# Kernel optimization log

Hardware: AMD Instinct MI355X
Metric: run time of the kernel (lower is better)

## Reference

```python
import jax, jax.numpy as jnp
import numpy as np

N = 50000
E = 200000
IN = 165
HID = 100
H1, H2, H3 = 8, 8, 1
NC = 2
DIM1 = HID * H1  # 800
DIM2 = HID * H2  # 800
NEG_SLOPE = 0.2


def setup_inputs() -> dict:
    key = jax.random.key(0)
    ks = jax.random.split(key, 20)
    p = lambda k, shape: jax.random.normal(k, shape, jnp.float32) * 0.05
    x = jax.random.normal(ks[0], (N, IN), jnp.float32)
    edge_index = jax.random.randint(ks[1], (2, E), 0, N, jnp.int64)
    return {
        "x": x,
        "edge_index": edge_index,
        "W1": p(ks[2], (IN, H1 * HID)), "a1s": p(ks[3], (H1, HID)),
        "a1d": p(ks[4], (H1, HID)), "b1": jnp.zeros((H1 * HID,), jnp.float32),
        "W2": p(ks[5], (DIM1, H2 * HID)), "a2s": p(ks[6], (H2, HID)),
        "a2d": p(ks[7], (H2, HID)), "b2": jnp.zeros((H2 * HID,), jnp.float32),
        # gat3: 800 -> 2, 1 head, mean (concat=False)
        "W3": p(ks[8], (DIM2, H3 * NC)), "a3s": p(ks[9], (H3, NC)),
        "a3d": p(ks[10], (H3, NC)), "b3": jnp.zeros((NC,), jnp.float32),
        # residual / skip linears (bias=False), stored [in, out]
        "Wres1": p(ks[11], (DIM1, DIM2)),
        "Wres2": p(ks[12], (DIM2, NC)),
        "Wskip": p(ks[13], (IN, NC)),
    }


def gat_conv(x, W, a_src, a_dst, b, src, dst, n, heads, ch, concat):
    # h: [n, heads, ch] projected node features
    h = (x @ W).reshape(n, heads, ch)
    e_src = (h * a_src).sum(-1)  # [n, heads]
    e_dst = (h * a_dst).sum(-1)
    # per-edge attention logits, LeakyReLU as in PyG GATConv
    e = jax.nn.leaky_relu(e_src[src] + e_dst[dst], NEG_SLOPE)  # [Etot, heads]
    # segment softmax over incoming edges of each destination node
    m = jax.ops.segment_max(e, dst, num_segments=n)
    ex = jnp.exp(e - m[dst])
    denom = jax.ops.segment_sum(ex, dst, num_segments=n)
    alpha = ex / (denom[dst] + 1e-16)
    # weighted scatter-aggregation of source messages
    out = jax.ops.segment_sum(alpha[:, :, None] * h[src], dst, num_segments=n)
    out = out.reshape(n, heads * ch) if concat else out.mean(axis=1)
    return out + b


def reference(x, edge_index, W1, a1s, a1d, b1, W2, a2s, a2d, b2,
              W3, a3s, a3d, b3, Wres1, Wres2, Wskip):
    n = x.shape[0]
    loop = jnp.arange(n, dtype=edge_index.dtype)  # PyG adds self-loops by default
    src = jnp.concatenate([edge_index[0], loop])
    dst = jnp.concatenate([edge_index[1], loop])

    h1 = jax.nn.elu(gat_conv(x, W1, a1s, a1d, b1, src, dst, n, H1, HID, True))
    h2 = gat_conv(h1, W2, a2s, a2d, b2, src, dst, n, H2, HID, True) + h1 @ Wres1
    h2 = jax.nn.elu(h2)
    logits = gat_conv(h2, W3, a3s, a3d, b3, src, dst, n, H3, NC, False)
    logits = logits + h2 @ Wres2 + x @ Wskip
    return logits
```

## Files before the change

kernel.cpp:

```cpp
#include <hip/hip_runtime.h>

#define NN     50000
#define NE     200000
#define ETOT   250000
#define FIN    165
#define KP1    192
#define HEADS  8
#define CH     100
#define DIM    800
#define MPAD   50048
#define NP1    896
#define DIM2   1600
#define NP2    1664
#define NEG    0.2f

typedef unsigned short u16;
typedef unsigned int   u32;
typedef __bf16 bf16x8 __attribute__((ext_vector_type(8)));
typedef float  f32x4  __attribute__((ext_vector_type(4)));

__device__ __forceinline__ u16 f2b(float f) {
  u32 u = __float_as_uint(f);
  u = (u + 0x7FFFu + ((u >> 16) & 1u)) >> 16;
  return (u16)u;
}
__device__ __forceinline__ float b2f(u16 u) { return __uint_as_float(((u32)u) << 16); }

__global__ void k_count(const int* __restrict__ ei, int* __restrict__ cnt) {
  int e = blockIdx.x * 256 + threadIdx.x;
  if (e >= ETOT) return;
  int d = (e < NE) ? ei[NE + e] : (e - NE);
  atomicAdd(&cnt[d], 1);
}
__global__ void k_bsum(const int* __restrict__ cnt, int* __restrict__ bs) {
  __shared__ int sm[256];
  int i = blockIdx.x * 256 + threadIdx.x;
  sm[threadIdx.x] = (i < NN) ? cnt[i] : 0;
  __syncthreads();
  for (int off = 128; off; off >>= 1) {
    if (threadIdx.x < off) sm[threadIdx.x] += sm[threadIdx.x + off];
    __syncthreads();
  }
  if (!threadIdx.x) bs[blockIdx.x] = sm[0];
}
__global__ void k_top(int* __restrict__ bs, int* __restrict__ rs, int nb) {
  __shared__ int sm[256];
  int t = threadIdx.x;
  int v = (t < nb) ? bs[t] : 0;
  sm[t] = v; __syncthreads();
  for (int off = 1; off < 256; off <<= 1) {
    int add = (t >= off) ? sm[t - off] : 0;
    __syncthreads();
    sm[t] += add;
    __syncthreads();
  }
  if (t < nb) bs[t] = sm[t] - v;
  if (!t) rs[NN] = ETOT;
}
__global__ void k_scan(const int* __restrict__ cnt, const int* __restrict__ bs, int* __restrict__ rs) {
  __shared__ int sm[256];
  int t = threadIdx.x, i = blockIdx.x * 256 + t;
  int v = (i < NN) ? cnt[i] : 0;
  sm[t] = v; __syncthreads();
  for (int off = 1; off < 256; off <<= 1) {
    int add = (t >= off) ? sm[t - off] : 0;
    __syncthreads();
    sm[t] += add;
    __syncthreads();
  }
  if (i < NN) rs[i] = bs[blockIdx.x] + sm[t] - v;
}
__global__ void k_fill(const int* __restrict__ ei, const int* __restrict__ rs,
                       int* __restrict__ cur, int* __restrict__ esrc) {
  int e = blockIdx.x * 256 + threadIdx.x;
  if (e >= ETOT) return;
  int s, d;
  if (e < NE) { s = ei[e]; d = ei[NE + e]; } else { s = d = e - NE; }
  int pos = atomicAdd(&cur[d], 1);
  esrc[rs[d] + pos] = s;
}

__global__ void k_cvt_x(const float* __restrict__ x, u16* __restrict__ A) {
  int idx = blockIdx.x * 256 + threadIdx.x;
  int r = idx / KP1, k = idx - r * KP1;
  float v = (r < NN && k < FIN) ? x[r * FIN + k] : 0.f;
  A[idx] = f2b(v);
}
__global__ void k_cvt_w1(const float* __restrict__ W1, u16* __restrict__ Bt) {
  int idx = blockIdx.x * 256 + threadIdx.x;
  int j = idx / KP1, k = idx - j * KP1;
  float v = (j < DIM && k < FIN) ? W1[k * DIM + j] : 0.f;
  Bt[idx] = f2b(v);
}
__global__ void k_cvt_w2(const float* __restrict__ W2, const float* __restrict__ Wr1,
                         u16* __restrict__ Bt) {
  int idx = blockIdx.x * 256 + threadIdx.x;
  int j = idx / DIM, k = idx - j * DIM;
  float v = 0.f;
  if (j < DIM) v = W2[k * DIM + j];
  else if (j < 2 * DIM) v = Wr1[k * DIM + (j - DIM)];
  Bt[idx] = f2b(v);
}
__global__ void k_wa(const float* __restrict__ W, const float* __restrict__ as,
                     const float* __restrict__ ad, u16* __restrict__ Wt,
                     int Kin, int Kpad, int Dsp) {
  int idx = blockIdx.x * 256 + threadIdx.x;
  if (idx >= 16 * Kpad) return;
  int j = idx / Kpad, k = idx - j * Kpad;
  int h = j & 7;
  const float* a = ((j < 8) ? as : ad) + h * CH;
  float s = 0.f;
  if (k < Kin) {
    const float* wr = W + (size_t)k * DIM + h * CH;
    for (int c = 0; c < CH; ++c) s += wr[c] * a[c];
  }
  Wt[(size_t)(Dsp + j) * Kpad + k] = f2b(s);
}

__device__ __forceinline__ void gl_lds16(const u16* g, u16* l) {
  __builtin_amdgcn_global_load_lds((const __attribute__((address_space(1))) void*)g,
                                   (__attribute__((address_space(3))) void*)l, 16, 0, 0);
}
#define WAITVM(N) asm volatile("s_waitcnt vmcnt(" #N ")" ::: "memory")

__global__ __launch_bounds__(256) void k_gemm(const u16* __restrict__ A, const u16* __restrict__ Bt,
                                              u16* __restrict__ C, float* __restrict__ es,
                                              float* __restrict__ ed, int ksteps, int K,
                                              int Dsplit, int Nreal, int ldC) {
  __shared__ __align__(16) u16 lA[3][128 * 32];
  __shared__ __align__(16) u16 lB[3][128 * 32];
  int t = threadIdx.x;
  int lane = t & 63, wv = t >> 6;

  int nwg = gridDim.x * gridDim.y;
  int h = blockIdx.y * gridDim.x + blockIdx.x;
  int q = nwg >> 3, r8 = nwg & 7;
  int xcd = h & 7, i8 = h >> 3;
  int ln = (xcd < r8 ? xcd * (q + 1) : r8 * (q + 1) + (xcd - r8) * q) + i8;
  int tn = (ln % gridDim.x) * 128, tm = (ln / gridDim.x) * 128;

  int wr = (wv >> 1) * 64, wc = (wv & 1) * 64;
  int rl = lane & 15, kl = (lane >> 4) * 8;
  int srow = t >> 2, scb = (t & 3) * 8;

  f32x4 acc[4][4];
#pragma unroll
  for (int i = 0; i < 4; ++i)
#pragma unroll
    for (int j = 0; j < 4; ++j) acc[i][j] = (f32x4){0.f, 0.f, 0.f, 0.f};

  auto stage = [&](int buf, int ks) {
    int k0 = ks * 32;
    gl_lds16(A  + (size_t)(tm + srow) * K + k0 + scb,       &lA[buf][t * 8]);
    gl_lds16(A  + (size_t)(tm + srow + 64) * K + k0 + scb,  &lA[buf][(256 + t) * 8]);
    gl_lds16(Bt + (size_t)(tn + srow) * K + k0 + scb,       &lB[buf][t * 8]);
    gl_lds16(Bt + (size_t)(tn + srow + 64) * K + k0 + scb,  &lB[buf][(256 + t) * 8]);
  };

  stage(0, 0);
  if (ksteps > 1) stage(1, 1);
  int cur = 0;
  for (int ks = 0; ks < ksteps; ++ks) {
    if (ks + 1 < ksteps) { WAITVM(4); } else { WAITVM(0); }
    __builtin_amdgcn_s_barrier();
    if (ks + 2 < ksteps) {
      int sb = (cur == 0) ? 2 : cur - 1;
      stage(sb, ks + 2);
    }
    bf16x8 af[4], bfr[4];
#pragma unroll
    for (int i = 0; i < 4; ++i) {
      af[i]  = *(const bf16x8*)&lA[cur][(wr + i * 16 + rl) * 32 + kl];
      bfr[i] = *(const bf16x8*)&lB[cur][(wc + i * 16 + rl) * 32 + kl];
    }
    __builtin_amdgcn_s_setprio(1);
#pragma unroll
    for (int i = 0; i < 4; ++i)
#pragma unroll
      for (int j = 0; j < 4; ++j)
        acc[i][j] = __builtin_amdgcn_mfma_f32_16x16x32_bf16(af[i], bfr[j], acc[i][j], 0, 0, 0);
    __builtin_amdgcn_s_setprio(0);
    cur = (cur == 2) ? 0 : cur + 1;
  }
  int rq = (lane >> 4) * 4;
#pragma unroll
  for (int i = 0; i < 4; ++i) {
#pragma unroll
    for (int j = 0; j < 4; ++j) {
      int col = tn + wc + j * 16 + rl;
      if (col < Dsplit) {
#pragma unroll
        for (int q2 = 0; q2 < 4; ++q2) {
          int row = tm + wr + i * 16 + rq + q2;
          C[(size_t)row * ldC + col] = f2b(acc[i][j][q2]);
        }
      } else if (col < Nreal) {
        int cj = col - Dsplit;
        float* dst = (cj < 8) ? es : ed;
        int hh = cj & 7;
#pragma unroll
        for (int q2 = 0; q2 < 4; ++q2) {
          int row = tm + wr + i * 16 + rq + q2;
          dst[(size_t)row * 8 + hh] = acc[i][j][q2];
        }
      }
    }
  }
}

__global__ void k_stats(const int* __restrict__ rs, const int* __restrict__ esrc,
                        const float* __restrict__ es, const float* __restrict__ ed,
                        float* __restrict__ ex, float* __restrict__ dv) {
  int idx = blockIdx.x * 256 + threadIdx.x;
  if (idx >= NN * HEADS) return;
  int n = idx >> 3, h = idx & 7;
  int beg = rs[n], end = rs[n + 1];
  float edv = ed[idx];
  float den = 0.f;
  for (int j = beg; j < end; ++j) {
    float x = es[esrc[j] * 8 + h] + edv;
    x = x > 0.f ? x : NEG * x;
    float e = __expf(x);
    ex[j * 8 + h] = e;
    den += e;
  }
  dv[idx] = 1.f / (den + 1e-16f);
}

template <int LAYER>
__global__ __launch_bounds__(256) void k_agg(const int* __restrict__ rs, const int* __restrict__ esrc,
    const u16* __restrict__ Hp, const float* __restrict__ ex, const float* __restrict__ dv,
    const float* __restrict__ bias, const u16* __restrict__ resid, u16* __restrict__ out) {
  const int ld = (LAYER == 2) ? DIM2 : DIM;
  int n = blockIdx.x, t = threadIdx.x;
  if (t >= 200) return;
  int beg = rs[n], end = rs[n + 1];
  int c = t * 4;
  int h = t / 25;
  float inv = dv[n * 8 + h];
  float a0 = 0.f, a1 = 0.f, a2 = 0.f, a3 = 0.f;
  for (int j = beg; j < end; ++j) {
    int s = esrc[j];
    float w = ex[j * 8 + h];
    ushort4 u = *(const ushort4*)(Hp + (size_t)s * ld + c);
    a0 += w * b2f(u.x); a1 += w * b2f(u.y); a2 += w * b2f(u.z); a3 += w * b2f(u.w);
  }
  const float4 bb = *(const float4*)(bias + c);
  float v0 = a0 * inv + bb.x, v1 = a1 * inv + bb.y, v2 = a2 * inv + bb.z, v3 = a3 * inv + bb.w;
  if (LAYER == 2) {
    ushort4 r = *(const ushort4*)(resid + (size_t)n * DIM2 + c);
    v0 += b2f(r.x); v1 += b2f(r.y); v2 += b2f(r.z); v3 += b2f(r.w);
  }
  v0 = v0 > 0.f ? v0 : __expf(v0) - 1.f;
  v1 = v1 > 0.f ? v1 : __expf(v1) - 1.f;
  v2 = v2 > 0.f ? v2 : __expf(v2) - 1.f;
  v3 = v3 > 0.f ? v3 : __expf(v3) - 1.f;
  ushort4 o;
  o.x = f2b(v0); o.y = f2b(v1); o.z = f2b(v2); o.w = f2b(v3);
  *(ushort4*)(out + (size_t)n * DIM + c) = o;
}

__global__ __launch_bounds__(256) void k_l3(const u16* __restrict__ h2, const float* __restrict__ x,
    const float* __restrict__ W3, const float* __restrict__ Wres2, const float* __restrict__ Wskip,
    const float* __restrict__ a3s, const float* __restrict__ a3d, const float* __restrict__ b3,
    float* __restrict__ H3p, float* __restrict__ base, float* __restrict__ es3, float* __restrict__ ed3) {
  int wv = threadIdx.x >> 6, lane = threadIdx.x & 63;
  int n = blockIdx.x * 4 + wv;
  if (n >= NN) return;
  float p0 = 0.f, p1 = 0.f, r0 = 0.f, r1 = 0.f;
  const u16* hr = h2 + (size_t)n * DIM;
  for (int c = lane; c < DIM; c += 64) {
    float v = b2f(hr[c]);
    p0 += v * W3[2 * c];    p1 += v * W3[2 * c + 1];
    r0 += v * Wres2[2 * c]; r1 += v * Wres2[2 * c + 1];
  }
  float s0 = 0.f, s1 = 0.f;
  const float* xr = x + (size_t)n * FIN;
  for (int c = lane; c < FIN; c += 64) {
    float v = xr[c];
    s0 += v * Wskip[2 * c]; s1 += v * Wskip[2 * c + 1];
  }
#pragma unroll
  for (int off = 32; off; off >>= 1) {
    p0 += __shfl_down(p0, off); p1 += __shfl_down(p1, off);
    r0 += __shfl_down(r0, off); r1 += __shfl_down(r1, off);
    s0 += __shfl_down(s0, off); s1 += __shfl_down(s1, off);
  }
  if (!lane) {
    H3p[2 * n] = p0; H3p[2 * n + 1] = p1;
    es3[n] = p0 * a3s[0] + p1 * a3s[1];
    ed3[n] = p0 * a3d[0] + p1 * a3d[1];
    base[2 * n]     = r0 + s0 + b3[0];
    base[2 * n + 1] = r1 + s1 + b3[1];
  }
}

__global__ void k_l3agg(const int* __restrict__ rs, const int* __restrict__ esrc,
                        const float* __restrict__ H3p, const float* __restrict__ base,
                        const float* __restrict__ es3, const float* __restrict__ ed3,
                        float* __restrict__ out) {
  int n = blockIdx.x * 256 + threadIdx.x;
  if (n >= NN) return;
  int beg = rs[n], end = rs[n + 1];
  float edv = ed3[n];
  float den = 0.f, a0 = 0.f, a1 = 0.f;
  for (int j = beg; j < end; ++j) {
    int s = esrc[j];
    float e = es3[s] + edv;
    e = e > 0.f ? e : NEG * e;
    float exv = __expf(e);
    den += exv;
    a0 += exv * H3p[2 * s];
    a1 += exv * H3p[2 * s + 1];
  }
  float inv = 1.f / (den + 1e-16f);
  out[2 * n]     = base[2 * n]     + a0 * inv;
  out[2 * n + 1] = base[2 * n + 1] + a1 * inv;
}

extern "C" void kernel_launch(void* const* d_in, const int* in_sizes, int n_in,
                              void* d_out, int out_size, void* d_ws, size_t ws_size,
                              hipStream_t stream) {
  (void)in_sizes; (void)n_in; (void)out_size; (void)ws_size;
  const float* x    = (const float*)d_in[0];
  const int*   ei   = (const int*)d_in[1];
  const float* W1   = (const float*)d_in[2];
  const float* a1s  = (const float*)d_in[3];
  const float* a1d  = (const float*)d_in[4];
  const float* b1   = (const float*)d_in[5];
  const float* W2   = (const float*)d_in[6];
  const float* a2s  = (const float*)d_in[7];
  const float* a2d  = (const float*)d_in[8];
  const float* b2   = (const float*)d_in[9];
  const float* W3   = (const float*)d_in[10];
  const float* a3s  = (const float*)d_in[11];
  const float* a3d  = (const float*)d_in[12];
  const float* b3   = (const float*)d_in[13];
  const float* Wr1  = (const float*)d_in[14];
  const float* Wr2  = (const float*)d_in[15];
  const float* Wsk  = (const float*)d_in[16];
  float* out = (float*)d_out;

  char* w = (char*)d_ws;
  size_t off = 0;
  auto alloc = [&](size_t bytes) { void* p = w + off; off += (bytes + 255) & ~(size_t)255; return p; };
  int* cnt   = (int*)alloc((size_t)NN * 4);
  int* cur   = (int*)alloc((size_t)NN * 4);
  int* rs    = (int*)alloc((size_t)(NN + 1) * 4);
  int* bs    = (int*)alloc(256 * 4);
  int* esrc  = (int*)alloc((size_t)ETOT * 4);
  float* es  = (float*)alloc((size_t)MPAD * HEADS * 4);
  float* ed  = (float*)alloc((size_t)MPAD * HEADS * 4);
  float* exb = (float*)alloc((size_t)ETOT * HEADS * 4);
  float* dvf = (float*)alloc((size_t)NN * HEADS * 4);
  u16* W1t   = (u16*)alloc((size_t)NP1 * KP1 * 2);
  u16* W2t   = (u16*)alloc((size_t)NP2 * DIM * 2);
  float* H3p = (float*)alloc((size_t)NN * 2 * 4);
  float* base= (float*)alloc((size_t)NN * 2 * 4);
  float* es3 = (float*)alloc((size_t)NN * 4);
  float* ed3 = (float*)alloc((size_t)NN * 4);
  u16* bufB  = (u16*)alloc((size_t)MPAD * DIM * 2);
  u16* bufA  = (u16*)alloc((size_t)MPAD * DIM2 * 2);
  u16* H1p   = bufA;
  u16* G2    = bufA;
  u16* A1    = bufA + (size_t)MPAD * DIM;

  const int nb = (NN + 255) / 256;
  const int ge = (ETOT + 255) / 256;
  const int gh = (NN * HEADS + 255) / 256;

  hipMemsetAsync(cnt, 0, (size_t)NN * 4, stream);
  hipMemsetAsync(cur, 0, (size_t)NN * 4, stream);
  k_count<<<ge, 256, 0, stream>>>(ei, cnt);
  k_bsum <<<nb, 256, 0, stream>>>(cnt, bs);
  k_top  <<<1, 256, 0, stream>>>(bs, rs, nb);
  k_scan <<<nb, 256, 0, stream>>>(cnt, bs, rs);
  k_fill <<<ge, 256, 0, stream>>>(ei, rs, cur, esrc);

  k_cvt_x <<<(MPAD * KP1) / 256, 256, 0, stream>>>(x, A1);
  k_cvt_w1<<<(NP1 * KP1) / 256, 256, 0, stream>>>(W1, W1t);
  k_wa    <<<(16 * KP1 + 255) / 256, 256, 0, stream>>>(W1, a1s, a1d, W1t, FIN, KP1, DIM);
  k_cvt_w2<<<(NP2 * DIM) / 256, 256, 0, stream>>>(W2, Wr1, W2t);
  k_wa    <<<(16 * DIM + 255) / 256, 256, 0, stream>>>(W2, a2s, a2d, W2t, DIM, DIM, DIM2);

  k_gemm<<<dim3(NP1 / 128, MPAD / 128), 256, 0, stream>>>(A1, W1t, H1p, es, ed,
                                                          KP1 / 32, KP1, DIM, DIM + 16, DIM);
  k_stats<<<gh, 256, 0, stream>>>(rs, esrc, es, ed, exb, dvf);
  k_agg<1><<<NN, 256, 0, stream>>>(rs, esrc, H1p, exb, dvf, b1, (const u16*)nullptr, bufB);

  k_gemm<<<dim3(NP2 / 128, MPAD / 128), 256, 0, stream>>>(bufB, W2t, G2, es, ed,
                                                          DIM / 32, DIM, DIM2, DIM2 + 16, DIM2);
  k_stats<<<gh, 256, 0, stream>>>(rs, esrc, es, ed, exb, dvf);
  k_agg<2><<<NN, 256, 0, stream>>>(rs, esrc, G2, exb, dvf, b2, G2 + DIM, bufB);

  k_l3   <<<(NN + 3) / 4, 256, 0, stream>>>(bufB, x, W3, Wr2, Wsk, a3s, a3d, b3, H3p, base, es3, ed3);
  k_l3agg<<<nb, 256, 0, stream>>>(rs, esrc, H3p, base, es3, ed3, out);
}
```

Measured before the change: 561.4 us.

## Replace 128x128 GEMM with 256x256 tile, 512-thread, swizzled LDS kernel

The bf16 MFMA GEMM moves from 128x128 tiles with K=32 steps and triple buffering to 256x256 tiles with 8 waves, K=64 steps and double buffering. The LDS layout is XOR-swizzled to avoid bank conflicts. Padding changes to fit the larger tiles: M goes to 50176, N to 1024/1792, and layer-2 K to 832. The workspace is reorganised, with row guards on stores, aliased buffers, and the layer-1 aggregation output written with the padded stride. The aim is more data reuse per tile and fewer LDS and global loads per MFMA, at the cost of more padded wasted compute and lower occupancy.

Measured after the change: 597.7 us. 6.5% more time.

```diff
diff --git a/kernel.cpp b/kernel.cpp
--- a/kernel.cpp
+++ b/kernel.cpp
@@ -8,10 +8,11 @@
 #define HEADS  8
 #define CH     100
 #define DIM    800
-#define MPAD   50048
-#define NP1    896
+#define MPAD   50176
+#define NP1    1024
 #define DIM2   1600
-#define NP2    1664
+#define KP2    832
+#define NP2    1792
 #define NEG    0.2f
 
 typedef unsigned short u16;
@@ -88,17 +89,18 @@
 }
 __global__ void k_cvt_w1(const float* __restrict__ W1, u16* __restrict__ Bt) {
   int idx = blockIdx.x * 256 + threadIdx.x;
+  if (idx >= DIM * KP1) return;
   int j = idx / KP1, k = idx - j * KP1;
-  float v = (j < DIM && k < FIN) ? W1[k * DIM + j] : 0.f;
+  float v = (k < FIN) ? W1[k * DIM + j] : 0.f;
   Bt[idx] = f2b(v);
 }
 __global__ void k_cvt_w2(const float* __restrict__ W2, const float* __restrict__ Wr1,
                          u16* __restrict__ Bt) {
   int idx = blockIdx.x * 256 + threadIdx.x;
-  int j = idx / DIM, k = idx - j * DIM;
+  if (idx >= DIM2 * KP2) return;
+  int j = idx / KP2, k = idx - j * KP2;
   float v = 0.f;
-  if (j < DIM) v = W2[k * DIM + j];
-  else if (j < 2 * DIM) v = Wr1[k * DIM + (j - DIM)];
+  if (k < DIM) v = (j < DIM) ? W2[k * DIM + j] : Wr1[k * DIM + (j - DIM)];
   Bt[idx] = f2b(v);
 }
 __global__ void k_wa(const float* __restrict__ W, const float* __restrict__ as,
@@ -123,76 +125,104 @@
 }
 #define WAITVM(N) asm volatile("s_waitcnt vmcnt(" #N ")" ::: "memory")
 
-__global__ __launch_bounds__(256) void k_gemm(const u16* __restrict__ A, const u16* __restrict__ Bt,
-                                              u16* __restrict__ C, float* __restrict__ es,
-                                              float* __restrict__ ed, int ksteps, int K,
-                                              int Dsplit, int Nreal, int ldC) {
-  __shared__ __align__(16) u16 lA[3][128 * 32];
-  __shared__ __align__(16) u16 lB[3][128 * 32];
-  int t = threadIdx.x;
-  int lane = t & 63, wv = t >> 6;
+__global__ __launch_bounds__(512, 2) void k_gemm256(
+    const u16* __restrict__ A, const u16* __restrict__ Bt, u16* __restrict__ C,
+    float* __restrict__ es, float* __restrict__ ed,
+    int Kpad, int NT, int Dsplit, int Nreal, int ldC, int Mreal) {
+  __shared__ __align__(16) u16 lA[2][16384];
+  __shared__ __align__(16) u16 lB[2][16384];
+  const int t = threadIdx.x;
+  const int lane = t & 63, w = t >> 6;
+  const int wm = w >> 2, wn = w & 3;
 
   int nwg = gridDim.x * gridDim.y;
-  int h = blockIdx.y * gridDim.x + blockIdx.x;
+  int hid = blockIdx.y * gridDim.x + blockIdx.x;
   int q = nwg >> 3, r8 = nwg & 7;
-  int xcd = h & 7, i8 = h >> 3;
+  int xcd = hid & 7, i8 = hid >> 3;
   int ln = (xcd < r8 ? xcd * (q + 1) : r8 * (q + 1) + (xcd - r8) * q) + i8;
-  int tn = (ln % gridDim.x) * 128, tm = (ln / gridDim.x) * 128;
-
-  int wr = (wv >> 1) * 64, wc = (wv & 1) * 64;
-  int rl = lane & 15, kl = (lane >> 4) * 8;
-  int srow = t >> 2, scb = (t & 3) * 8;
-
-  f32x4 acc[4][4];
-#pragma unroll
-  for (int i = 0; i < 4; ++i)
+  int tn = (ln % gridDim.x) * 256, tm = (ln / gridDim.x) * 256;
+
+  const int srow = ((w >> 1) << 4) + (lane >> 2);
+  const int scol = ((w & 1) << 5) + (((lane & 3) * 8) ^ (((lane >> 5) & 1) << 4));
+  const size_t rA = (size_t)(tm + srow) * Kpad + scol;
+  const size_t rB = (size_t)(tn + srow) * Kpad + scol;
+  const size_t oR = (size_t)64 * Kpad;
+  const int dul = w * 512 + lane * 8;
+
+  f32x4 acc[8][4];
+#pragma unroll
+  for (int i = 0; i < 8; ++i)
 #pragma unroll
     for (int j = 0; j < 4; ++j) acc[i][j] = (f32x4){0.f, 0.f, 0.f, 0.f};
 
-  auto stage = [&](int buf, int ks) {
-    int k0 = ks * 32;
-    gl_lds16(A  + (size_t)(tm + srow) * K + k0 + scb,       &lA[buf][t * 8]);
-    gl_lds16(A  + (size_t)(tm + srow + 64) * K + k0 + scb,  &lA[buf][(256 + t) * 8]);
-    gl_lds16(Bt + (size_t)(tn + srow) * K + k0 + scb,       &lB[buf][t * 8]);
-    gl_lds16(Bt + (size_t)(tn + srow + 64) * K + k0 + scb,  &lB[buf][(256 + t) * 8]);
+  auto issue = [&](int buf, int kt) {
+    const u16* pa = A + rA + (size_t)kt * 64;
+    gl_lds16(pa,          &lA[buf][dul]);
+    gl_lds16(pa + oR,     &lA[buf][4096 + dul]);
+    gl_lds16(pa + 2 * oR, &lA[buf][8192 + dul]);
+    gl_lds16(pa + 3 * oR, &lA[buf][12288 + dul]);
+    const u16* pb = Bt + rB + (size_t)kt * 64;
+    gl_lds16(pb,          &lB[buf][dul]);
+    gl_lds16(pb + oR,     &lB[buf][4096 + dul]);
+    gl_lds16(pb + 2 * oR, &lB[buf][8192 + dul]);
+    gl_lds16(pb + 3 * oR, &lB[buf][12288 + dul]);
   };
 
-  stage(0, 0);
-  if (ksteps > 1) stage(1, 1);
-  int cur = 0;
-  for (int ks = 0; ks < ksteps; ++ks) {
-    if (ks + 1 < ksteps) { WAITVM(4); } else { WAITVM(0); }
+  const int rl = lane & 15, kl = (lane >> 4) * 8;
+  const int rdoff = rl * 32 + (kl ^ (((rl >> 3) & 1) << 4));
+
+  issue(0, 0);
+  if (NT > 1) issue(1, 1);
+  WAITVM(8);
+  __builtin_amdgcn_s_barrier();
+
+  for (int kt = 0; kt < NT; ++kt) {
+    const int buf = kt & 1;
+    const u16* baseA = &lA[buf][wm * 8192];
+    const u16* baseB = &lB[buf][(wn >> 1) * 8192];
+    bf16x8 b[4][2];
+#pragma unroll
+    for (int fc = 0; fc < 4; ++fc)
+#pragma unroll
+      for (int kk = 0; kk < 2; ++kk)
+        b[fc][kk] = *(const bf16x8*)&baseB[((((wn & 1) * 4 + fc) * 2 + kk) << 9) + rdoff];
+#pragma unroll
+    for (int qm = 0; qm < 2; ++qm) {
+      bf16x8 a[4][2];
+#pragma unroll
+      for (int i = 0; i < 4; ++i)
+#pragma unroll
+        for (int kk = 0; kk < 2; ++kk)
+          a[i][kk] = *(const bf16x8*)&baseA[((((qm * 4 + i) * 2) + kk) << 9) + rdoff];
+      __builtin_amdgcn_s_setprio(1);
+#pragma unroll
+      for (int i = 0; i < 4; ++i)
+#pragma unroll
+        for (int fc = 0; fc < 4; ++fc)
+#pragma unroll
+          for (int kk = 0; kk < 2; ++kk)
+            acc[qm * 4 + i][fc] =
+                __builtin_amdgcn_mfma_f32_16x16x32_bf16(a[i][kk], b[fc][kk], acc[qm * 4 + i][fc], 0, 0, 0);
+      __builtin_amdgcn_s_setprio(0);
+    }
     __builtin_amdgcn_s_barrier();
-    if (ks + 2 < ksteps) {
-      int sb = (cur == 0) ? 2 : cur - 1;
-      stage(sb, ks + 2);
-    }
-    bf16x8 af[4], bfr[4];
-#pragma unroll
-    for (int i = 0; i < 4; ++i) {
-      af[i]  = *(const bf16x8*)&lA[cur][(wr + i * 16 + rl) * 32 + kl];
-      bfr[i] = *(const bf16x8*)&lB[cur][(wc + i * 16 + rl) * 32 + kl];
-    }
-    __builtin_amdgcn_s_setprio(1);
-#pragma unroll
-    for (int i = 0; i < 4; ++i)
-#pragma unroll
-      for (int j = 0; j < 4; ++j)
-        acc[i][j] = __builtin_amdgcn_mfma_f32_16x16x32_bf16(af[i], bfr[j], acc[i][j], 0, 0, 0);
-    __builtin_amdgcn_s_setprio(0);
-    cur = (cur == 2) ? 0 : cur + 1;
-  }
-  int rq = (lane >> 4) * 4;
-#pragma unroll
-  for (int i = 0; i < 4; ++i) {
-#pragma unroll
-    for (int j = 0; j < 4; ++j) {
-      int col = tn + wc + j * 16 + rl;
+    if (kt + 2 < NT) { issue(buf, kt + 2); WAITVM(8); }
+    else             { WAITVM(0); }
+    __builtin_amdgcn_s_barrier();
+    __builtin_amdgcn_sched_barrier(0);
+  }
+
+  const int rq = (lane >> 4) * 4;
+#pragma unroll
+  for (int fr = 0; fr < 8; ++fr) {
+#pragma unroll
+    for (int fc = 0; fc < 4; ++fc) {
+      int col = tn + wn * 64 + fc * 16 + rl;
       if (col < Dsplit) {
 #pragma unroll
         for (int q2 = 0; q2 < 4; ++q2) {
-          int row = tm + wr + i * 16 + rq + q2;
-          C[(size_t)row * ldC + col] = f2b(acc[i][j][q2]);
+          int row = tm + wm * 128 + fr * 16 + rq + q2;
+          if (row < Mreal) C[(size_t)row * ldC + col] = f2b(acc[fr][fc][q2]);
         }
       } else if (col < Nreal) {
         int cj = col - Dsplit;
@@ -200,8 +230,8 @@
         int hh = cj & 7;
 #pragma unroll
         for (int q2 = 0; q2 < 4; ++q2) {
-          int row = tm + wr + i * 16 + rq + q2;
-          dst[(size_t)row * 8 + hh] = acc[i][j][q2];
+          int row = tm + wm * 128 + fr * 16 + rq + q2;
+          if (row < Mreal) dst[(size_t)row * 8 + hh] = acc[fr][fc][q2];
         }
       }
     }
@@ -231,7 +261,8 @@
 __global__ __launch_bounds__(256) void k_agg(const int* __restrict__ rs, const int* __restrict__ esrc,
     const u16* __restrict__ Hp, const float* __restrict__ ex, const float* __restrict__ dv,
     const float* __restrict__ bias, const u16* __restrict__ resid, u16* __restrict__ out) {
-  const int ld = (LAYER == 2) ? DIM2 : DIM;
+  const int ld  = (LAYER == 2) ? DIM2 : DIM;
+  const int old = (LAYER == 1) ? KP2 : DIM;
   int n = blockIdx.x, t = threadIdx.x;
   if (t >= 200) return;
   int beg = rs[n], end = rs[n + 1];
@@ -241,9 +272,9 @@
   float a0 = 0.f, a1 = 0.f, a2 = 0.f, a3 = 0.f;
   for (int j = beg; j < end; ++j) {
     int s = esrc[j];
-    float w = ex[j * 8 + h];
+    float wv = ex[j * 8 + h];
     ushort4 u = *(const ushort4*)(Hp + (size_t)s * ld + c);
-    a0 += w * b2f(u.x); a1 += w * b2f(u.y); a2 += w * b2f(u.z); a3 += w * b2f(u.w);
+    a0 += wv * b2f(u.x); a1 += wv * b2f(u.y); a2 += wv * b2f(u.z); a3 += wv * b2f(u.w);
   }
   const float4 bb = *(const float4*)(bias + c);
   float v0 = a0 * inv + bb.x, v1 = a1 * inv + bb.y, v2 = a2 * inv + bb.z, v3 = a3 * inv + bb.w;
@@ -257,7 +288,7 @@
   v3 = v3 > 0.f ? v3 : __expf(v3) - 1.f;
   ushort4 o;
   o.x = f2b(v0); o.y = f2b(v1); o.z = f2b(v2); o.w = f2b(v3);
-  *(ushort4*)(out + (size_t)n * DIM + c) = o;
+  *(ushort4*)(out + (size_t)n * old + c) = o;
 }
 
 __global__ __launch_bounds__(256) void k_l3(const u16* __restrict__ h2, const float* __restrict__ x,
@@ -349,21 +380,21 @@
   int* rs    = (int*)alloc((size_t)(NN + 1) * 4);
   int* bs    = (int*)alloc(256 * 4);
   int* esrc  = (int*)alloc((size_t)ETOT * 4);
-  float* es  = (float*)alloc((size_t)MPAD * HEADS * 4);
-  float* ed  = (float*)alloc((size_t)MPAD * HEADS * 4);
+  float* es  = (float*)alloc((size_t)NN * HEADS * 4);
+  float* ed  = (float*)alloc((size_t)NN * HEADS * 4);
   float* exb = (float*)alloc((size_t)ETOT * HEADS * 4);
   float* dvf = (float*)alloc((size_t)NN * HEADS * 4);
-  u16* W1t   = (u16*)alloc((size_t)NP1 * KP1 * 2);
-  u16* W2t   = (u16*)alloc((size_t)NP2 * DIM * 2);
-  float* H3p = (float*)alloc((size_t)NN * 2 * 4);
-  float* base= (float*)alloc((size_t)NN * 2 * 4);
-  float* es3 = (float*)alloc((size_t)NN * 4);
-  float* ed3 = (float*)alloc((size_t)NN * 4);
-  u16* bufB  = (u16*)alloc((size_t)MPAD * DIM * 2);
-  u16* bufA  = (u16*)alloc((size_t)MPAD * DIM2 * 2);
+  u16* W2t   = (u16*)alloc((size_t)NP2 * KP2 * 2);
+  u16* bufB  = (u16*)alloc((size_t)MPAD * KP2 * 2);
+  u16* bufA  = (u16*)alloc((size_t)NN * DIM2 * 2);
   u16* H1p   = bufA;
+  u16* A1    = bufA + (size_t)NN * DIM;
+  u16* W1t   = A1 + (size_t)MPAD * KP1;
   u16* G2    = bufA;
-  u16* A1    = bufA + (size_t)MPAD * DIM;
+  float* H3p  = exb;
+  float* base = exb + 2 * NN;
+  float* es3  = exb + 4 * NN;
+  float* ed3  = exb + 5 * NN;
 
   const int nb = (NN + 255) / 256;
   const int ge = (ETOT + 255) / 256;
@@ -378,18 +409,18 @@
   k_fill <<<ge, 256, 0, stream>>>(ei, rs, cur, esrc);
 
   k_cvt_x <<<(MPAD * KP1) / 256, 256, 0, stream>>>(x, A1);
-  k_cvt_w1<<<(NP1 * KP1) / 256, 256, 0, stream>>>(W1, W1t);
-  k_wa    <<<(16 * KP1 + 255) / 256, 256, 0, stream>>>(W1, a1s, a1d, W1t, FIN, KP1, DIM);
-  k_cvt_w2<<<(NP2 * DIM) / 256, 256, 0, stream>>>(W2, Wr1, W2t);
-  k_wa    <<<(16 * DIM + 255) / 256, 256, 0, stream>>>(W2, a2s, a2d, W2t, DIM, DIM, DIM2);
-
-  k_gemm<<<dim3(NP1 / 128, MPAD / 128), 256, 0, stream>>>(A1, W1t, H1p, es, ed,
-                                                          KP1 / 32, KP1, DIM, DIM + 16, DIM);
+  k_cvt_w1<<<(DIM * KP1) / 256, 256, 0, stream>>>(W1, W1t);
+  k_wa    <<<(16 * KP1) / 256, 256, 0, stream>>>(W1, a1s, a1d, W1t, FIN, KP1, DIM);
+  k_cvt_w2<<<(DIM2 * KP2) / 256, 256, 0, stream>>>(W2, Wr1, W2t);
+  k_wa    <<<(16 * KP2) / 256, 256, 0, stream>>>(W2, a2s, a2d, W2t, DIM, KP2, DIM2);
+
+  k_gemm256<<<dim3(NP1 / 256, MPAD / 256), 512, 0, stream>>>(
+      A1, W1t, H1p, es, ed, KP1, KP1 / 64, DIM, DIM + 16, DIM, NN);
   k_stats<<<gh, 256, 0, stream>>>(rs, esrc, es, ed, exb, dvf);
   k_agg<1><<<NN, 256, 0, stream>>>(rs, esrc, H1p, exb, dvf, b1, (const u16*)nullptr, bufB);
 
-  k_gemm<<<dim3(NP2 / 128, MPAD / 128), 256, 0, stream>>>(bufB, W2t, G2, es, ed,
-                                                          DIM / 32, DIM, DIM2, DIM2 + 16, DIM2);
+  k_gemm256<<<dim3(NP2 / 256, MPAD / 256), 512, 0, stream>>>(
+      bufB, W2t, G2, es, ed, KP2, KP2 / 64, DIM2, DIM2 + 16, DIM2, NN);
   k_stats<<<gh, 256, 0, stream>>>(rs, esrc, es, ed, exb, dvf);
   k_agg<2><<<NN, 256, 0, stream>>>(rs, esrc, G2, exb, dvf, b2, G2 + DIM, bufB);
 
```
